# Optimization experiments

Hardware: AMD Instinct MI355X
Metric: run time of the kernel (lower is better)

Reference implementation:

```python
import jax, jax.numpy as jnp
import numpy as np

T, B, S, D = 512, 32, 512, 512
EPS = 1e-6  # LayerNorm eps


def _ln(x, g, b):
    m = jnp.mean(x, axis=-1, keepdims=True)
    v = jnp.mean((x - m) ** 2, axis=-1, keepdims=True)
    return g * (x - m) * jax.lax.rsqrt(v + EPS) + b


def setup_inputs() -> dict:
    key = jax.random.key(0)
    ks = jax.random.split(key, 10)
    sc = 1.0 / np.sqrt(D).astype(np.float32)
    return {
        "prev_layer": jax.random.normal(ks[0], (T, B, D), jnp.float32),
        "hidden": jax.random.normal(ks[1], (B, D), jnp.float32),
        "enc_output": jax.random.normal(ks[2], (B, S, D), jnp.float32),
        "memory_length": jax.random.randint(ks[3], (B,), 1, S + 1),
        # nn.Linear weights stored as [in, out] (transposed torch layout)
        "W_in": jax.random.normal(ks[4], (D, 3 * D), jnp.float32) * sc,
        "W_enc": jax.random.normal(ks[5], (D, D), jnp.float32) * sc,
        "W_attn_in": jax.random.normal(ks[6], (D, D), jnp.float32) * sc,
        "W_hidden": jax.random.normal(ks[7], (D, D), jnp.float32) * sc,
        "W_ctx": jax.random.normal(ks[8], (D, D), jnp.float32) * sc,
        # LayerNorm gains/biases (5 LNs)
        "g_pre": jnp.ones((3 * D,), jnp.float32), "b_pre": jnp.zeros((3 * D,), jnp.float32),
        "g_enc": jnp.ones((D,), jnp.float32), "b_enc": jnp.zeros((D,), jnp.float32),
        "g_attn": jnp.ones((D,), jnp.float32), "b_attn": jnp.zeros((D,), jnp.float32),
        "g_h": jnp.ones((D,), jnp.float32), "b_h": jnp.zeros((D,), jnp.float32),
        "g_c": jnp.ones((D,), jnp.float32), "b_c": jnp.zeros((D,), jnp.float32),
    }


def reference(prev_layer, hidden, enc_output, W_in, W_enc, W_attn_in, W_hidden,
              W_ctx, g_pre, b_pre, g_enc, b_enc, g_attn, b_attn, g_h, b_h,
              g_c, b_c, memory_length):
    d = prev_layer.shape[-1]
    sqrt_d = jnp.sqrt(jnp.asarray(d, prev_layer.dtype))
    # dropout is identity in eval mode
    preact = _ln(prev_layer @ W_in, g_pre, b_pre)          # [T,B,3D]
    pctx = _ln(enc_output @ W_enc, g_enc, b_enc)           # [B,S,D]
    z, h_gate, pl_t = jnp.split(preact, 3, axis=-1)
    z = jax.nn.sigmoid(z)
    h_gate = jax.nn.sigmoid(h_gate)

    # SRU-style linear recurrence: s_t = (1-z_t)*s_{t-1} + z_t*pl_t
    def step(h, zp):
        z_t, p_t = zp
        s = (1.0 - z_t) * h + z_t * p_t
        return s, s

    hidden_last, ss = jax.lax.scan(step, hidden, (z, pl_t))  # ss: [T,B,D]

    attn_in = _ln(ss @ W_attn_in, g_attn, b_attn)            # [T,B,D]
    align = jnp.einsum('tbd,bsd->bts', attn_in, pctx)        # [B,T,S]
    mask = jnp.arange(pctx.shape[1])[None, :] < memory_length[:, None]  # [B,S]
    align = jnp.where(mask[:, None, :], align, -jnp.inf)
    av = jax.nn.softmax(align / sqrt_d, axis=-1)             # [B,T,S]
    c = jnp.einsum('bts,bsd->tbd', av, pctx)                 # [T,B,D]
    attn_out = c / sqrt_d

    trans = _ln(ss @ W_hidden, g_h, b_h) + _ln(attn_out @ W_ctx, g_c, b_c)
    out = jnp.tanh(trans)
    out = (1.0 - h_gate) * out + h_gate * prev_layer         # [T,B,D]
    p_attn = jnp.transpose(av, (1, 0, 2))                    # [T,B,S]
    return out, hidden_last, p_attn
```

## Files before the change

kernel.cpp:

```cpp
#include <hip/hip_runtime.h>
#include <hip/hip_bf16.h>
#include <cmath>

#define T_ 512
#define B_ 32
#define S_ 512
#define D_ 512
#define D3_ 1536
#define NCH 16
#define CT (T_ / NCH)
static constexpr float LN_EPS = 1e-6f;
static constexpr float RSQRT_D = 0.044194173824159216f;

typedef __attribute__((ext_vector_type(8))) __bf16 bf16x8;
typedef __attribute__((ext_vector_type(4))) float f32x4;

struct __align__(8) bfx4 { __hip_bfloat16 x, y, z, w; };

__device__ __forceinline__ void g2l16(const void* g, void* l) {
    __builtin_amdgcn_global_load_lds(
        (const __attribute__((address_space(1))) unsigned int*)g,
        (__attribute__((address_space(3))) unsigned int*)l, 16, 0, 0);
}

__device__ __forceinline__ float xr_sum16(float v) {
    v += __shfl_xor(v, 1); v += __shfl_xor(v, 2);
    v += __shfl_xor(v, 4); v += __shfl_xor(v, 8); return v;
}
__device__ __forceinline__ float xr_max16(float v) {
    v = fmaxf(v, __shfl_xor(v, 1)); v = fmaxf(v, __shfl_xor(v, 2));
    v = fmaxf(v, __shfl_xor(v, 4)); v = fmaxf(v, __shfl_xor(v, 8)); return v;
}

__device__ __forceinline__ float sigmoidf_(float x) {
    return 1.f / (1.f + __expf(-x));
}
__device__ __forceinline__ float sigmoid_fast(float x) {
    return __fdividef(1.f, 1.f + __expf(-x));
}
__device__ __forceinline__ float tanh_fast(float x) {
    return 1.f - __fdividef(2.f, __expf(2.f * x) + 1.f);
}
__device__ __forceinline__ float bfu(unsigned short u) {
    unsigned int v = ((unsigned int)u) << 16;
    return __uint_as_float(v);
}

__global__ __launch_bounds__(256) void gemm_pre(
    const __hip_bfloat16* __restrict__ A,
    const __hip_bfloat16* __restrict__ Bw,
    __hip_bfloat16* __restrict__ preb,
    float2* __restrict__ part)
{
    __shared__ char smem[16384];
    __hip_bfloat16* As = (__hip_bfloat16*)smem;
    __hip_bfloat16* Bs = (__hip_bfloat16*)(smem + 8192);

    const int m0 = blockIdx.y * 128, n0 = blockIdx.x * 128;
    const int tid = threadIdx.x, lane = tid & 63, w = tid >> 6;
    const int wm = (w >> 1) * 64, wn = (w & 1) * 64;
    const int srow = lane >> 2, skB = (lane & 3) * 16;
    const int q = lane >> 4, c = lane & 15;

    f32x4 acc[4][4];
#pragma unroll
    for (int i = 0; i < 4; i++)
#pragma unroll
        for (int j = 0; j < 4; j++) acc[i][j] = (f32x4)(0.0f);

    const char* ga0 = (const char*)(A + (long)(m0 + w * 16 + srow) * 512) + skB;
    const char* ga1 = (const char*)(A + (long)(m0 + (w + 4) * 16 + srow) * 512) + skB;
    const char* gb0 = (const char*)(Bw + (long)(n0 + w * 16 + srow) * 512) + skB;
    const char* gb1 = (const char*)(Bw + (long)(n0 + (w + 4) * 16 + srow) * 512) + skB;
    char* la0 = (char*)As + w * 1024 + lane * 16;
    char* la1 = (char*)As + (w + 4) * 1024 + lane * 16;
    char* lb0 = (char*)Bs + w * 1024 + lane * 16;
    char* lb1 = (char*)Bs + (w + 4) * 1024 + lane * 16;
    const char* Ar = (const char*)As + (wm + c) * 64 + q * 16;
    const char* Br = (const char*)Bs + (wn + c) * 64 + q * 16;

    for (int k0 = 0; k0 < 512; k0 += 32) {
        const long kb = (long)k0 * 2;
        g2l16(ga0 + kb, la0);
        g2l16(ga1 + kb, la1);
        g2l16(gb0 + kb, lb0);
        g2l16(gb1 + kb, lb1);
        __syncthreads();
        bf16x8 af[4], bfr[4];
#pragma unroll
        for (int i = 0; i < 4; i++) {
            af[i] = *(const bf16x8*)(Ar + i * 1024);
            bfr[i] = *(const bf16x8*)(Br + i * 1024);
        }
#pragma unroll
        for (int i = 0; i < 4; i++)
#pragma unroll
            for (int j = 0; j < 4; j++)
                acc[i][j] = __builtin_amdgcn_mfma_f32_16x16x32_bf16(
                    af[i], bfr[j], acc[i][j], 0, 0, 0);
        __syncthreads();
    }

    float2* sred = (float2*)smem;
#pragma unroll
    for (int i = 0; i < 4; i++)
#pragma unroll
        for (int r = 0; r < 4; r++) {
            float s = 0.f, qq = 0.f;
#pragma unroll
            for (int j = 0; j < 4; j++) {
                float v = acc[i][j][r]; s += v; qq += v * v;
            }
            s = xr_sum16(s); qq = xr_sum16(qq);
            if (c == 0) sred[(wm + i * 16 + q * 4 + r) * 2 + (w & 1)] =
                make_float2(s, qq);
        }
    __syncthreads();
    if ((w & 1) == 0 && c == 0) {
#pragma unroll
        for (int i = 0; i < 4; i++)
#pragma unroll
            for (int r = 0; r < 4; r++) {
                int row = wm + i * 16 + q * 4 + r;
                float2 a = sred[row * 2], b2 = sred[row * 2 + 1];
                part[(long)blockIdx.x * 16384 + m0 + row] =
                    make_float2(a.x + b2.x, a.y + b2.y);
            }
    }
    __syncthreads();

    for (int p = 0; p < 2; p++) {
        if ((w >> 1) == p) {
#pragma unroll
            for (int i = 0; i < 4; i++)
#pragma unroll
                for (int j = 0; j < 4; j++)
#pragma unroll
                    for (int r = 0; r < 4; r++) {
                        int row = i * 16 + q * 4 + r;
                        int col = wn + j * 16 + c;
                        ((__hip_bfloat16*)smem)[row * 128 + col] =
                            __float2bfloat16(acc[i][j][r]);
                    }
        }
        __syncthreads();
#pragma unroll
        for (int rnd = 0; rnd < 4; rnd++) {
            int row = rnd * 16 + (tid >> 4);
            int ch = tid & 15;
            uint4 v = *(const uint4*)(smem + row * 256 + ch * 16);
            long grow = m0 + p * 64 + row;
            *(uint4*)((char*)preb + grow * 3072 + (long)n0 * 2 + ch * 16) = v;
        }
        __syncthreads();
    }
}

#define RC_BUF 34816
__device__ __forceinline__ void rows_core32(
    const __hip_bfloat16* A, long lda,
    const __hip_bfloat16* B, long ldb,
    char* smem, f32x4 (&acc)[2][8])
{
    const int tid = threadIdx.x, lane = tid & 63, w = tid >> 6;
#pragma unroll
    for (int m = 0; m < 2; m++)
#pragma unroll
        for (int j = 0; j < 8; j++) acc[m][j] = (f32x4)(0.0f);

    const char* ga = (const char*)(A + (long)(w * 16 + (lane >> 2)) * lda) + (lane & 3) * 16;
    char* la = smem + w * 1024 + lane * 16;
    const char* gb = (const char*)(B + (long)(w * 128 + (lane >> 2)) * ldb) + (lane & 3) * 16;
    char* lb = smem + 2048 + w * 8192 + lane * 16;
    const long ldbB16 = (long)ldb * 32;
    const char* Ar = smem + (lane & 15) * 64 + (lane >> 4) * 16;
    const char* Br = smem + 2048 + (w * 128 + (lane & 15)) * 64 + (lane >> 4) * 16;

    if (w < 2) g2l16(ga, la);
#pragma unroll
    for (int s = 0; s < 8; s++) g2l16(gb + s * ldbB16, lb + s * 1024);
    __syncthreads();

#pragma unroll
    for (int kk = 0; kk < 16; kk++) {
        const int cb = (kk & 1) * RC_BUF;
        const int nb = ((kk & 1) ^ 1) * RC_BUF;
        if (kk < 15) {
            const long kb = (long)(kk + 1) * 64;
            if (w < 2) g2l16(ga + kb, la + nb);
#pragma unroll
            for (int s = 0; s < 8; s++)
                g2l16(gb + kb + s * ldbB16, lb + nb + s * 1024);
        }
        bf16x8 af[2], bfr[8];
#pragma unroll
        for (int m = 0; m < 2; m++) af[m] = *(const bf16x8*)(Ar + cb + m * 1024);
#pragma unroll
        for (int j = 0; j < 8; j++) bfr[j] = *(const bf16x8*)(Br + cb + j * 1024);
#pragma unroll
        for (int m = 0; m < 2; m++)
#pragma unroll
            for (int j = 0; j < 8; j++)
                acc[m][j] = __builtin_amdgcn_mfma_f32_16x16x32_bf16(
                    af[m], bfr[j], acc[m][j], 0, 0, 0);
        __syncthreads();
    }
}

__global__ __launch_bounds__(256, 2) void gemm_ln(
    const __hip_bfloat16* __restrict__ A, long lda,
    const __hip_bfloat16* __restrict__ W,
    const float* __restrict__ g, const float* __restrict__ bb,
    __hip_bfloat16* __restrict__ out)
{
    __shared__ char smem[69632];
    const long m0 = (long)blockIdx.y * 32;
    f32x4 acc[2][8];
    rows_core32(A + m0 * lda, lda, W, 512, smem, acc);

    const int tid = threadIdx.x, lane = tid & 63, w = tid >> 6;
    const int q = lane >> 4, c = lane & 15;
    float2* sred = (float2*)smem;
#pragma unroll
    for (int m = 0; m < 2; m++)
#pragma unroll
        for (int r = 0; r < 4; r++) {
            float s = 0.f, qq = 0.f;
#pragma unroll
            for (int j = 0; j < 8; j++) {
                float v = acc[m][j][r]; s += v; qq += v * v;
            }
            s = xr_sum16(s); qq = xr_sum16(qq);
            if (c == 0) sred[(m * 16 + q * 4 + r) * 4 + w] = make_float2(s, qq);
        }
    __syncthreads();
    float mean[2][4], rstd[2][4];
#pragma unroll
    for (int m = 0; m < 2; m++)
#pragma unroll
        for (int r = 0; r < 4; r++) {
            int row = m * 16 + q * 4 + r;
            float s = 0.f, qq = 0.f;
#pragma unroll
            for (int ww = 0; ww < 4; ww++) {
                float2 t = sred[row * 4 + ww]; s += t.x; qq += t.y;
            }
            float mn = s * (1.f / 512);
            mean[m][r] = mn;
            rstd[m][r] = rsqrtf(qq * (1.f / 512) - mn * mn + LN_EPS);
        }
    __syncthreads();
#pragma unroll
    for (int m = 0; m < 2; m++)
#pragma unroll
        for (int j = 0; j < 8; j++) {
            int col = w * 128 + j * 16 + c;
            float gv = g[col], bv = bb[col];
#pragma unroll
            for (int r = 0; r < 4; r++) {
                int row = m * 16 + q * 4 + r;
                float v = (acc[m][j][r] - mean[m][r]) * rstd[m][r] * gv + bv;
                ((__hip_bfloat16*)smem)[row * 512 + col] = __float2bfloat16(v);
            }
        }
    __syncthreads();
#pragma unroll
    for (int rnd = 0; rnd < 8; rnd++) {
        int row = rnd * 4 + w;
        uint4 v = *(const uint4*)(smem + row * 1024 + lane * 16);
        *(uint4*)((char*)out + (m0 + row) * 1024 + lane * 16) = v;
    }
}

__global__ __launch_bounds__(256, 2) void gemm_attn(
    const __hip_bfloat16* __restrict__ attninb,
    const __hip_bfloat16* __restrict__ pctxb,
    const int* __restrict__ mlen,
    float* __restrict__ pattn, __hip_bfloat16* __restrict__ pattnb)
{
    __shared__ char smem[69632];
    const int b = blockIdx.z;
    const long t0 = (long)blockIdx.y * 32;
    f32x4 acc[2][8];
    rows_core32(attninb + (long)b * 512 + t0 * 16384, 16384,
                pctxb + (long)b * 262144, 512, smem, acc);

    const int tid = threadIdx.x, lane = tid & 63, w = tid >> 6;
    const int q = lane >> 4, c = lane & 15;
    const int len = mlen[b];
    float* sred = (float*)smem;

#pragma unroll
    for (int m = 0; m < 2; m++)
#pragma unroll
        for (int r = 0; r < 4; r++) {
            float mx = -INFINITY;
#pragma unroll
            for (int j = 0; j < 8; j++) {
                int col = w * 128 + j * 16 + c;
                float v = acc[m][j][r] * RSQRT_D;
                acc[m][j][r] = v;
                if (col < len) mx = fmaxf(mx, v);
            }
            mx = xr_max16(mx);
            if (c == 0) sred[(m * 16 + q * 4 + r) * 4 + w] = mx;
        }
    __syncthreads();
    float rmax[2][4];
#pragma unroll
    for (int m = 0; m < 2; m++)
#pragma unroll
        for (int r = 0; r < 4; r++) {
            int row = m * 16 + q * 4 + r;
            rmax[m][r] = fmaxf(fmaxf(sred[row * 4], sred[row * 4 + 1]),
                               fmaxf(sred[row * 4 + 2], sred[row * 4 + 3]));
        }
    __syncthreads();
#pragma unroll
    for (int m = 0; m < 2; m++)
#pragma unroll
        for (int r = 0; r < 4; r++) {
            float s = 0.f;
#pragma unroll
            for (int j = 0; j < 8; j++) {
                int col = w * 128 + j * 16 + c;
                float e = (col < len) ? __expf(acc[m][j][r] - rmax[m][r]) : 0.f;
                acc[m][j][r] = e; s += e;
            }
            s = xr_sum16(s);
            if (c == 0) sred[(m * 16 + q * 4 + r) * 4 + w] = s;
        }
    __syncthreads();
    float rinv[2][4];
#pragma unroll
    for (int m = 0; m < 2; m++)
#pragma unroll
        for (int r = 0; r < 4; r++) {
            int row = m * 16 + q * 4 + r;
            rinv[m][r] = 1.f / (sred[row * 4] + sred[row * 4 + 1] +
                                sred[row * 4 + 2] + sred[row * 4 + 3]);
        }
    __syncthreads();

#pragma unroll
    for (int m = 0; m < 2; m++)
#pragma unroll
        for (int j = 0; j < 8; j++)
#pragma unroll
            for (int r = 0; r < 4; r++) {
                int row = m * 16 + q * 4 + r;
                int col = w * 128 + j * 16 + c;
                float p = acc[m][j][r] * rinv[m][r];
                acc[m][j][r] = p;
                pattn[((t0 + row) * 32 + b) * 512 + col] = p;
                ((__hip_bfloat16*)smem)[row * 512 + col] = __float2bfloat16(p);
            }
    __syncthreads();
#pragma unroll
    for (int rnd = 0; rnd < 8; rnd++) {
        int row = rnd * 4 + w;
        uint4 v = *(const uint4*)(smem + row * 1024 + lane * 16);
        *(uint4*)((char*)pattnb + ((t0 + row) * 32 + b) * 1024 + lane * 16) = v;
    }
}

__global__ __launch_bounds__(256, 2) void gemm_av(
    const __hip_bfloat16* __restrict__ pattnb,
    const __hip_bfloat16* __restrict__ pctxT,
    __hip_bfloat16* __restrict__ attnoutb)
{
    __shared__ char smem[69632];
    const int b = blockIdx.z;
    const long t0 = (long)blockIdx.y * 32;
    f32x4 acc[2][8];
    rows_core32(pattnb + (long)b * 512 + t0 * 16384, 16384,
                pctxT + (long)b * 262144, 512, smem, acc);

    const int tid = threadIdx.x, lane = tid & 63, w = tid >> 6;
    const int q = lane >> 4, c = lane & 15;
#pragma unroll
    for (int m = 0; m < 2; m++)
#pragma unroll
        for (int j = 0; j < 8; j++)
#pragma unroll
            for (int r = 0; r < 4; r++) {
                int row = m * 16 + q * 4 + r;
                int col = w * 128 + j * 16 + c;
                ((__hip_bfloat16*)smem)[row * 512 + col] =
                    __float2bfloat16(acc[m][j][r] * RSQRT_D);
            }
    __syncthreads();
#pragma unroll
    for (int rnd = 0; rnd < 8; rnd++) {
        int row = rnd * 4 + w;
        uint4 v = *(const uint4*)(smem + row * 1024 + lane * 16);
        *(uint4*)((char*)attnoutb + ((t0 + row) * 32 + b) * 1024 + lane * 16) = v;
    }
}

__global__ __launch_bounds__(256, 2) void gemm_fin(
    const __hip_bfloat16* __restrict__ attnoutb,
    const __hip_bfloat16* __restrict__ Wc,
    const __hip_bfloat16* __restrict__ h1n,
    const __hip_bfloat16* __restrict__ preb,
    const float2* __restrict__ stats,
    const float* __restrict__ g_c, const float* __restrict__ b_c,
    const float* __restrict__ g_pre, const float* __restrict__ b_pre,
    const float* __restrict__ prev, float* __restrict__ out)
{
    __shared__ char smem[69632];
    const long m0 = (long)blockIdx.y * 32;
    f32x4 acc[2][8];
    rows_core32(attnoutb + m0 * 512, 512, Wc, 512, smem, acc);

    const int tid = threadIdx.x, lane = tid & 63, w = tid >> 6;
    const int q = lane >> 4, c = lane & 15;
    float2* sred = (float2*)smem;
#pragma unroll
    for (int m = 0; m < 2; m++)
#pragma unroll
        for (int r = 0; r < 4; r++) {
            float s = 0.f, qq = 0.f;
#pragma unroll
            for (int j = 0; j < 8; j++) {
                float v = acc[m][j][r]; s += v; qq += v * v;
            }
            s = xr_sum16(s); qq = xr_sum16(qq);
            if (c == 0) sred[(m * 16 + q * 4 + r) * 4 + w] = make_float2(s, qq);
        }
    __syncthreads();
    float mean[2][4], rstd[2][4];
#pragma unroll
    for (int m = 0; m < 2; m++)
#pragma unroll
        for (int r = 0; r < 4; r++) {
            int row = m * 16 + q * 4 + r;
            float s = 0.f, qq = 0.f;
#pragma unroll
            for (int ww = 0; ww < 4; ww++) {
                float2 t = sred[row * 4 + ww]; s += t.x; qq += t.y;
            }
            float mn = s * (1.f / 512);
            mean[m][r] = mn;
            rstd[m][r] = rsqrtf(qq * (1.f / 512) - mn * mn + LN_EPS);
        }
    __syncthreads();

    float* t2s = (float*)smem;
#pragma unroll
    for (int m = 0; m < 2; m++)
#pragma unroll
        for (int j = 0; j < 8; j++) {
            int col = w * 128 + j * 16 + c;
            float gv = g_c[col], bv = b_c[col];
#pragma unroll
            for (int r = 0; r < 4; r++) {
                int row = m * 16 + q * 4 + r;
                t2s[row * 512 + col] =
                    (acc[m][j][r] - mean[m][r]) * rstd[m][r] * gv + bv;
            }
        }
    __syncthreads();

#pragma unroll
    for (int ch = 0; ch < 16; ch++) {
        int f4 = ch * 256 + tid;
        int row = f4 >> 7;
        long rowg = m0 + row;
        int col = (f4 & 127) * 4;
        float4 t2 = ((const float4*)t2s)[f4];
        ushort4 h1 = *(const ushort4*)((const char*)h1n + rowg * 1024 + col * 2);
        ushort4 hr = *(const ushort4*)((const char*)preb + rowg * 3072 + 1024 + col * 2);
        float4 pv = *(const float4*)(prev + rowg * 512 + col);
        float4 gp = *(const float4*)(g_pre + 512 + col);
        float4 bp = *(const float4*)(b_pre + 512 + col);
        float2 sh = stats[rowg];
        auto fuse = [&](unsigned short h1u, unsigned short hru, float t2v,
                        float pvv, float gpv, float bpv) -> float {
            float hg = sigmoid_fast((bfu(hru) - sh.x) * sh.y * gpv + bpv);
            float th = tanh_fast(bfu(h1u) + t2v);
            return (1.f - hg) * th + hg * pvv;
        };
        float4 o;
        o.x = fuse(h1.x, hr.x, t2.x, pv.x, gp.x, bp.x);
        o.y = fuse(h1.y, hr.y, t2.y, pv.y, gp.y, bp.y);
        o.z = fuse(h1.z, hr.z, t2.z, pv.z, gp.z, bp.z);
        o.w = fuse(h1.w, hr.w, t2.w, pv.w, gp.w, bp.w);
        *(float4*)(out + rowg * 512 + col) = o;
    }
}

__global__ __launch_bounds__(256) void cvt4(
    const float* __restrict__ x, __hip_bfloat16* __restrict__ y, int n4)
{
    int i = blockIdx.x * 256 + threadIdx.x;
    if (i >= n4) return;
    float4 v = ((const float4*)x)[i];
    bfx4 o;
    o.x = __float2bfloat16(v.x); o.y = __float2bfloat16(v.y);
    o.z = __float2bfloat16(v.z); o.w = __float2bfloat16(v.w);
    ((bfx4*)y)[i] = o;
}

__global__ __launch_bounds__(256) void wtrans(
    const float* __restrict__ w0, const float* __restrict__ w1,
    const float* __restrict__ w2, const float* __restrict__ w3,
    const float* __restrict__ w4, __hip_bfloat16* __restrict__ WT)
{
    int z = blockIdx.z;
    const float* W; long off; int N;
    if (z == 0)      { W = w0; off = 0;                N = 1536; }
    else if (z == 1) { W = w1; off = 786432;           N = 512; }
    else if (z == 2) { W = w2; off = 786432 + 262144;  N = 512; }
    else if (z == 3) { W = w3; off = 786432 + 524288;  N = 512; }
    else             { W = w4; off = 786432 + 786432;  N = 512; }
    int n0 = blockIdx.x * 32, k0 = blockIdx.y * 32;
    if (n0 >= N) return;
    __shared__ float t[32][33];
    int tx = threadIdx.x & 31, ty = threadIdx.x >> 5;
#pragma unroll
    for (int i = 0; i < 4; i++)
        t[ty + i * 8][tx] = W[(long)(k0 + ty + i * 8) * N + n0 + tx];
    __syncthreads();
    __hip_bfloat16* O = WT + off;
#pragma unroll
    for (int i = 0; i < 4; i++)
        O[(long)(n0 + ty + i * 8) * 512 + k0 + tx] =
            __float2bfloat16(t[tx][ty + i * 8]);
}

__global__ __launch_bounds__(256) void ptrans(
    const __hip_bfloat16* __restrict__ src, __hip_bfloat16* __restrict__ dst)
{
    long boff = (long)blockIdx.z * (S_ * D_);
    int d0 = blockIdx.x * 32, s0 = blockIdx.y * 32;
    __shared__ __hip_bfloat16 t[32][34];
    int tx = threadIdx.x & 31, ty = threadIdx.x >> 5;
#pragma unroll
    for (int i = 0; i < 4; i++)
        t[ty + i * 8][tx] = src[boff + (long)(s0 + ty + i * 8) * D_ + d0 + tx];
    __syncthreads();
#pragma unroll
    for (int i = 0; i < 4; i++)
        dst[boff + (long)(d0 + ty + i * 8) * S_ + s0 + tx] = t[tx][ty + i * 8];
}

__global__ __launch_bounds__(256) void stats_fin(
    const float2* __restrict__ part, float2* __restrict__ stats)
{
    int r = blockIdx.x * 256 + threadIdx.x;
    float s = 0.f, qq = 0.f;
#pragma unroll
    for (int cb = 0; cb < 12; cb++) {
        float2 v = part[(long)cb * 16384 + r]; s += v.x; qq += v.y;
    }
    float m = s * (1.f / 1536);
    float rs = rsqrtf(qq * (1.f / 1536) - m * m + LN_EPS);
    stats[r] = make_float2(m, rs);
}

__global__ __launch_bounds__(256) void scan_part1(
    const __hip_bfloat16* __restrict__ preb, const float2* __restrict__ stats,
    const float* __restrict__ gpre, const float* __restrict__ bpre,
    float* __restrict__ Ap, float* __restrict__ Bp)
{
    int idx = blockIdx.x * 256 + threadIdx.x;
    int b = idx >> 9, d = idx & 511;
    int ch = blockIdx.y;
    float gz = gpre[d], bz = bpre[d];
    float gp = gpre[1024 + d], bpv = bpre[1024 + d];
    float A = 1.f, s = 0.f;
    for (int t = ch * CT; t < (ch + 1) * CT; t++) {
        long row = (long)t * 32 + b;
        float2 st = stats[row];
        float zr = __bfloat162float(preb[row * 1536 + d]);
        float pr = __bfloat162float(preb[row * 1536 + 1024 + d]);
        float z = sigmoidf_((zr - st.x) * st.y * gz + bz);
        float pl = (pr - st.x) * st.y * gp + bpv;
        float a = 1.f - z;
        A *= a;
        s = a * s + z * pl;
    }
    Ap[ch * 16384 + idx] = A;
    Bp[ch * 16384 + idx] = s;
}

__global__ __launch_bounds__(256) void scan_part2(
    const float* __restrict__ Ap, const float* __restrict__ Bp,
    const float* __restrict__ h0, float* __restrict__ sin_,
    float* __restrict__ hlast)
{
    int idx = blockIdx.x * 256 + threadIdx.x;
    float s = h0[idx];
    for (int ch = 0; ch < NCH; ch++) {
        sin_[ch * 16384 + idx] = s;
        s = Ap[ch * 16384 + idx] * s + Bp[ch * 16384 + idx];
    }
    hlast[idx] = s;
}

__global__ __launch_bounds__(256) void scan_part3(
    const __hip_bfloat16* __restrict__ preb, const float2* __restrict__ stats,
    const float* __restrict__ gpre, const float* __restrict__ bpre,
    const float* __restrict__ sin_, __hip_bfloat16* __restrict__ ssb)
{
    int idx = blockIdx.x * 256 + threadIdx.x;
    int b = idx >> 9, d = idx & 511;
    int ch = blockIdx.y;
    float gz = gpre[d], bz = bpre[d];
    float gp = gpre[1024 + d], bpv = bpre[1024 + d];
    float s = sin_[ch * 16384 + idx];
    for (int t = ch * CT; t < (ch + 1) * CT; t++) {
        long row = (long)t * 32 + b;
        float2 st = stats[row];
        float zr = __bfloat162float(preb[row * 1536 + d]);
        float pr = __bfloat162float(preb[row * 1536 + 1024 + d]);
        float z = sigmoidf_((zr - st.x) * st.y * gz + bz);
        float pl = (pr - st.x) * st.y * gp + bpv;
        s += z * (pl - s);
        ssb[(long)t * 16384 + idx] = __float2bfloat16(s);
    }
}

extern "C" void kernel_launch(void* const* d_in, const int* in_sizes, int n_in,
                              void* d_out, int out_size, void* d_ws, size_t ws_size,
                              hipStream_t stream) {
    const float* prev  = (const float*)d_in[0];
    const float* hid0  = (const float*)d_in[1];
    const float* enc   = (const float*)d_in[2];
    const int*   mlen  = (const int*)  d_in[3];
    const float* W_in  = (const float*)d_in[4];
    const float* W_enc = (const float*)d_in[5];
    const float* W_att = (const float*)d_in[6];
    const float* W_hid = (const float*)d_in[7];
    const float* W_ctx = (const float*)d_in[8];
    const float* g_pre = (const float*)d_in[9];
    const float* b_pre = (const float*)d_in[10];
    const float* g_enc = (const float*)d_in[11];
    const float* b_enc = (const float*)d_in[12];
    const float* g_att = (const float*)d_in[13];
    const float* b_att = (const float*)d_in[14];
    const float* g_h   = (const float*)d_in[15];
    const float* b_h   = (const float*)d_in[16];
    const float* g_c   = (const float*)d_in[17];
    const float* b_c   = (const float*)d_in[18];

    float* out   = (float*)d_out;
    float* hlast = out + (long)T_ * B_ * D_;
    float* pattn = hlast + (long)B_ * D_;

    char* ws = (char*)d_ws;
    __hip_bfloat16* preb    = (__hip_bfloat16*)(ws);
    __hip_bfloat16* WT      = (__hip_bfloat16*)(ws + 50331648);
    __hip_bfloat16* prevb   = (__hip_bfloat16*)(ws + 54525952);
    __hip_bfloat16* encb    = (__hip_bfloat16*)(ws + 71303168);
    __hip_bfloat16* pctxb   = (__hip_bfloat16*)(ws + 88080384);
    __hip_bfloat16* pctxT   = (__hip_bfloat16*)(ws + 104857600);
    __hip_bfloat16* ssb     = (__hip_bfloat16*)(ws + 121634816);
    __hip_bfloat16* attninb = (__hip_bfloat16*)(ws + 138412032);
    __hip_bfloat16* pattnb  = (__hip_bfloat16*)(ws + 155189248);
    __hip_bfloat16* attnoutb= (__hip_bfloat16*)(ws + 171966464);
    __hip_bfloat16* h1n     = (__hip_bfloat16*)(ws + 188743680);
    float2* part            = (float2*)(ws + 205520896);
    float2* stats           = (float2*)(ws + 207093760);
    float* scanA            = (float*)(ws + 207224832);
    float* scanB            = (float*)(ws + 208273408);
    float* sinb             = (float*)(ws + 209321984);

    const __hip_bfloat16* W_encT = WT + 786432;
    const __hip_bfloat16* W_attT = WT + 786432 + 262144;
    const __hip_bfloat16* W_hidT = WT + 786432 + 524288;
    const __hip_bfloat16* W_ctxT = WT + 786432 + 786432;

    dim3 blk(256);

    cvt4<<<8192, blk, 0, stream>>>(prev, prevb, 2097152);
    cvt4<<<8192, blk, 0, stream>>>(enc, encb, 2097152);
    wtrans<<<dim3(48, 16, 5), blk, 0, stream>>>(W_in, W_enc, W_att, W_hid,
                                                W_ctx, WT);

    gemm_pre<<<dim3(12, 128), blk, 0, stream>>>(prevb, WT, preb, part);
    stats_fin<<<64, blk, 0, stream>>>(part, stats);

    scan_part1<<<dim3(64, NCH), blk, 0, stream>>>(preb, stats, g_pre, b_pre,
                                                  scanA, scanB);
    scan_part2<<<64, blk, 0, stream>>>(scanA, scanB, hid0, sinb, hlast);
    scan_part3<<<dim3(64, NCH), blk, 0, stream>>>(preb, stats, g_pre, b_pre,
                                                  sinb, ssb);

    gemm_ln<<<dim3(1, 512), blk, 0, stream>>>(encb, 512, W_encT, g_enc, b_enc,
                                              pctxb);
    ptrans<<<dim3(16, 16, 32), blk, 0, stream>>>(pctxb, pctxT);

    gemm_ln<<<dim3(1, 512), blk, 0, stream>>>(ssb, 512, W_attT, g_att, b_att,
                                              attninb);

    gemm_attn<<<dim3(1, 16, 32), blk, 0, stream>>>(attninb, pctxb, mlen,
                                                   pattn, pattnb);

    gemm_av<<<dim3(1, 16, 32), blk, 0, stream>>>(pattnb, pctxT, attnoutb);

    gemm_ln<<<dim3(1, 512), blk, 0, stream>>>(ssb, 512, W_hidT, g_h, b_h, h1n);

    gemm_fin<<<dim3(1, 512), blk, 0, stream>>>(attnoutb, W_ctxT, h1n, preb,
                                               stats, g_c, b_c, g_pre, b_pre,
                                               prev, out);
}
```

Baseline: 444.4 us.

## Double-buffer LDS tiles and swizzle block order in pre-activation GEMM

Doubles the shared memory of the prev_layer @ W_in GEMM to hold two K-stage buffers, so the next tile's global-to-LDS load is issued before the MFMAs on the current tile, overlapping memory with compute. It also remaps the linear block index with a swizzle so that blocks running at the same time share A/B tiles in cache. The cost is 32KB of LDS per block, which may lower occupancy, plus the index arithmetic. The part[] index now uses the swizzled column block.

```diff
diff --git a/kernel.cpp b/kernel.cpp
--- a/kernel.cpp
+++ b/kernel.cpp
@@ -52,11 +52,12 @@
     __hip_bfloat16* __restrict__ preb,
     float2* __restrict__ part)
 {
-    __shared__ char smem[16384];
-    __hip_bfloat16* As = (__hip_bfloat16*)smem;
-    __hip_bfloat16* Bs = (__hip_bfloat16*)(smem + 8192);
-
-    const int m0 = blockIdx.y * 128, n0 = blockIdx.x * 128;
+    __shared__ char smem[32768];
+
+    const int lin = blockIdx.y * 12 + blockIdx.x;
+    const int swz = (lin & 7) * 192 + (lin >> 3);
+    const int bx = swz % 12, by = swz / 12;
+    const int m0 = by * 128, n0 = bx * 128;
     const int tid = threadIdx.x, lane = tid & 63, w = tid >> 6;
     const int wm = (w >> 1) * 64, wn = (w & 1) * 64;
     const int srow = lane >> 2, skB = (lane & 3) * 16;
@@ -72,25 +73,35 @@
     const char* ga1 = (const char*)(A + (long)(m0 + (w + 4) * 16 + srow) * 512) + skB;
     const char* gb0 = (const char*)(Bw + (long)(n0 + w * 16 + srow) * 512) + skB;
     const char* gb1 = (const char*)(Bw + (long)(n0 + (w + 4) * 16 + srow) * 512) + skB;
-    char* la0 = (char*)As + w * 1024 + lane * 16;
-    char* la1 = (char*)As + (w + 4) * 1024 + lane * 16;
-    char* lb0 = (char*)Bs + w * 1024 + lane * 16;
-    char* lb1 = (char*)Bs + (w + 4) * 1024 + lane * 16;
-    const char* Ar = (const char*)As + (wm + c) * 64 + q * 16;
-    const char* Br = (const char*)Bs + (wn + c) * 64 + q * 16;
-
-    for (int k0 = 0; k0 < 512; k0 += 32) {
-        const long kb = (long)k0 * 2;
-        g2l16(ga0 + kb, la0);
-        g2l16(ga1 + kb, la1);
-        g2l16(gb0 + kb, lb0);
-        g2l16(gb1 + kb, lb1);
-        __syncthreads();
+    char* la0 = smem + w * 1024 + lane * 16;
+    char* la1 = smem + (w + 4) * 1024 + lane * 16;
+    char* lb0 = smem + 8192 + w * 1024 + lane * 16;
+    char* lb1 = smem + 8192 + (w + 4) * 1024 + lane * 16;
+    const char* Ar = smem + (wm + c) * 64 + q * 16;
+    const char* Br = smem + 8192 + (wn + c) * 64 + q * 16;
+
+    g2l16(ga0, la0);
+    g2l16(ga1, la1);
+    g2l16(gb0, lb0);
+    g2l16(gb1, lb1);
+    __syncthreads();
+
+#pragma unroll
+    for (int kk = 0; kk < 16; kk++) {
+        const int cb = (kk & 1) << 14;
+        const int nb = cb ^ 16384;
+        if (kk < 15) {
+            const long kb = (long)(kk + 1) * 64;
+            g2l16(ga0 + kb, la0 + nb);
+            g2l16(ga1 + kb, la1 + nb);
+            g2l16(gb0 + kb, lb0 + nb);
+            g2l16(gb1 + kb, lb1 + nb);
+        }
         bf16x8 af[4], bfr[4];
 #pragma unroll
         for (int i = 0; i < 4; i++) {
-            af[i] = *(const bf16x8*)(Ar + i * 1024);
-            bfr[i] = *(const bf16x8*)(Br + i * 1024);
+            af[i] = *(const bf16x8*)(Ar + cb + i * 1024);
+            bfr[i] = *(const bf16x8*)(Br + cb + i * 1024);
         }
 #pragma unroll
         for (int i = 0; i < 4; i++)
@@ -123,7 +134,7 @@
             for (int r = 0; r < 4; r++) {
                 int row = wm + i * 16 + q * 4 + r;
                 float2 a = sred[row * 2], b2 = sred[row * 2 + 1];
-                part[(long)blockIdx.x * 16384 + m0 + row] =
+                part[(long)bx * 16384 + m0 + row] =
                     make_float2(a.x + b2.x, a.y + b2.y);
             }
     }
```

Result: no change. 436.4 us (-1.8%).
